# Optimization experiments

Measured on AMD Instinct MI355X. Metric: run time of the kernel, lower is better.

The kernel has to match this reference:

```python
import jax, jax.numpy as jnp
import numpy as np

B, S, D, E, K = 4, 2048, 1024, 8, 2
H = 4 * D  # SwiGLU hidden size


def setup_inputs() -> dict:
    key = jax.random.key(0)
    ks = jax.random.split(key, 6)
    s = 0.02
    return {
        "x": jax.random.normal(ks[0], (B, S, D), dtype=jnp.float32),
        "Wr": jax.random.normal(ks[1], (D, E), dtype=jnp.float32) * s,
        "br": jnp.zeros((E,), jnp.float32),
        "Wg": jax.random.normal(ks[2], (E, D, H), dtype=jnp.float32) * s,
        "bg": jnp.zeros((E, H), jnp.float32),
        "Wu": jax.random.normal(ks[3], (E, D, H), dtype=jnp.float32) * s,
        "bu": jnp.zeros((E, H), jnp.float32),
        "Wd": jax.random.normal(ks[4], (E, H, D), dtype=jnp.float32) * s,
        "bd": jnp.zeros((E, D), jnp.float32),
        "top_k": K,
    }


def reference(x, Wr, br, Wg, bg, Wu, bu, Wd, bd, top_k):
    # Router: top-k over expert logits, softmax over the selected k values.
    Bx, Sx, Dx = x.shape
    Ex = Wr.shape[-1]
    logits = x @ Wr + br                              # [B,S,E]
    vals, idx = jax.lax.top_k(logits, top_k)          # [B,S,K]
    probs = jax.nn.softmax(vals, axis=-1)             # [B,S,K]
    # Dense per-token expert weight; 0 for experts the token is not routed to.
    gate_w = jnp.sum(jax.nn.one_hot(idx, Ex, dtype=x.dtype) * probs[..., None], axis=-2)  # [B,S,E]

    xt = x.reshape(-1, Dx)          # [T,D]
    gw = gate_w.reshape(-1, Ex).T   # [E,T]

    def body(acc, p):
        wg, bgi, wu, bui, wd, bdi, ge = p
        h = jax.nn.silu(xt @ wg + bgi) * (xt @ wu + bui)   # [T,4D]
        y = (h @ wd + bdi) * ge[:, None]                   # zero where ge==0 (not routed)
        return acc + y, None

    out, _ = jax.lax.scan(body, jnp.zeros_like(xt), (Wg, bg, Wu, bu, Wd, bd, gw))
    return out.reshape(Bx, Sx, Dx)
```

## Files before the change

kernel.cpp:

```cpp
#include <hip/hip_runtime.h>
#include <hip/hip_fp16.h>


#define T_TOK 8192
#define D_IN  1024
#define E_EXP 8
#define H_HID 4096
#define NSLOT (T_TOK * 2)
#define NSLOT_PAD (NSLOT + 256)

typedef _Float16 f16;
typedef __attribute__((ext_vector_type(8))) _Float16 f16x8;
typedef __attribute__((ext_vector_type(4))) _Float16 f16x4;
typedef __attribute__((ext_vector_type(4))) float f32x4;

__device__ __forceinline__ void gload_lds16(const void* g, void* l) {
  __builtin_amdgcn_global_load_lds(
      (const __attribute__((address_space(1))) unsigned int*)g,
      (__attribute__((address_space(3))) unsigned int*)l, 16, 0, 0);
}


__global__ __launch_bounds__(256) void convert_x_kernel(
    const float* __restrict__ x, f16* __restrict__ xb, int n4) {
  int i = blockIdx.x * 256 + threadIdx.x;
  if (i >= n4) return;
  float4 v = ((const float4*)x)[i];
  f16x4 o = {(f16)v.x, (f16)v.y, (f16)v.z, (f16)v.w};
  *(f16x4*)(xb + (size_t)i * 4) = o;
}

template<int MAP>
__global__ __launch_bounds__(256) void transpose_cvt_kernel(
    const float* __restrict__ src, f16* __restrict__ dst, int R, int C,
    size_t dstride) {
  __shared__ float tile[32][33];
  int b = blockIdx.z;
  const float* s = src + (size_t)b * R * C;
  f16* d = dst + (size_t)b * dstride;
  int c0 = blockIdx.x * 32, r0 = blockIdx.y * 32;
  int tr = threadIdx.x >> 3;
  int tc4 = (threadIdx.x & 7) * 4;
  float4 v = *(const float4*)(s + (size_t)(r0 + tr) * C + c0 + tc4);
  tile[tr][tc4 + 0] = v.x;
  tile[tr][tc4 + 1] = v.y;
  tile[tr][tc4 + 2] = v.z;
  tile[tr][tc4 + 3] = v.w;
  __syncthreads();
  int c = c0 + tr;
  int ro = (MAP == 0) ? c : (((c >> 4) << 5) + ((MAP == 2) ? 16 : 0) + (c & 15));
  f16x4 o = {(f16)tile[tc4 + 0][tr], (f16)tile[tc4 + 1][tr],
             (f16)tile[tc4 + 2][tr], (f16)tile[tc4 + 3][tr]};
  *(f16x4*)(d + (size_t)ro * R + r0 + tc4) = o;
}


__global__ __launch_bounds__(256) void router_kernel(
    const float* __restrict__ x, const float* __restrict__ Wr,
    const float* __restrict__ br, int* __restrict__ eidx,
    float2* __restrict__ pval, int* __restrict__ counts) {
  int lane = threadIdx.x & 63, wid = threadIdx.x >> 6;
  int t = blockIdx.x * 4 + wid;
  const float* xr = x + (size_t)t * D_IN;
  float s[8] = {0.f, 0.f, 0.f, 0.f, 0.f, 0.f, 0.f, 0.f};
  int dbase = lane * 16;
#pragma unroll
  for (int i = 0; i < 4; ++i) {
    float4 xv = *(const float4*)(xr + dbase + i * 4);
    const float xs[4] = {xv.x, xv.y, xv.z, xv.w};
#pragma unroll
    for (int j = 0; j < 4; ++j) {
      const float* wr = Wr + (size_t)(dbase + i * 4 + j) * E_EXP;
      float4 w0 = *(const float4*)wr;
      float4 w1 = *(const float4*)(wr + 4);
      float xvj = xs[j];
      s[0] += xvj * w0.x; s[1] += xvj * w0.y; s[2] += xvj * w0.z; s[3] += xvj * w0.w;
      s[4] += xvj * w1.x; s[5] += xvj * w1.y; s[6] += xvj * w1.z; s[7] += xvj * w1.w;
    }
  }
#pragma unroll
  for (int off = 32; off; off >>= 1)
#pragma unroll
    for (int e = 0; e < 8; ++e) s[e] += __shfl_xor(s[e], off);
  if (lane == 0) {
    float v[8];
#pragma unroll
    for (int e = 0; e < 8; ++e) v[e] = s[e] + br[e];
    int i0 = 0; float v0 = v[0];
#pragma unroll
    for (int e = 1; e < 8; ++e) if (v[e] > v0) { v0 = v[e]; i0 = e; }
    int i1 = -1; float v1 = -1e30f;
#pragma unroll
    for (int e = 0; e < 8; ++e)
      if (e != i0 && v[e] > v1) { v1 = v[e]; i1 = e; }
    float ed = __expf(v1 - v0);
    float inv = 1.f / (1.f + ed);
    eidx[t] = i0 | (i1 << 8);
    pval[t] = make_float2(inv, ed * inv);
    atomicAdd(&counts[i0], 1);
    atomicAdd(&counts[i1], 1);
  }
}

__global__ void scan_kernel(const int* __restrict__ counts, int* __restrict__ offsets) {
  if (threadIdx.x == 0) {
    int acc = 0;
#pragma unroll
    for (int e = 0; e < E_EXP; ++e) { offsets[e] = acc; acc += counts[e]; }
    offsets[E_EXP] = acc;
  }
}

__global__ __launch_bounds__(256) void scatter_kernel(
    const int* __restrict__ eidx, const float2* __restrict__ pval,
    const int* __restrict__ offsets, int* __restrict__ cursors,
    int* __restrict__ perm, float* __restrict__ gatew, int2* __restrict__ slotAB) {
  int t = blockIdx.x * 256 + threadIdx.x;
  if (t >= T_TOK) return;
  int ei = eidx[t];
  float2 p = pval[t];
  int e0 = ei & 0xff, e1 = (ei >> 8) & 0xff;
  int s0 = offsets[e0] + atomicAdd(&cursors[e0], 1);
  perm[s0] = t; gatew[s0] = p.x;
  int s1 = offsets[e1] + atomicAdd(&cursors[e1], 1);
  perm[s1] = t; gatew[s1] = p.y;
  slotAB[t] = make_int2(s0, s1);
}


#define SB0 __builtin_amdgcn_sched_barrier(0)
#define BAR do { SB0; __builtin_amdgcn_s_barrier(); SB0; } while (0)

#define STAGE_(B, ISB, H, KT, BASE) do {                                   \
  char* d_ = smem + (B)*65536 + (ISB)*32768 + (H)*16384 + wid*1024;        \
  gload_lds16(BASE[(H)*2+0] + (size_t)(KT)*64, d_);                        \
  gload_lds16(BASE[(H)*2+1] + (size_t)(KT)*64, d_ + 8192);                 \
} while (0)

#define LDA_(B, Q)                                                          \
  _Pragma("unroll")                                                         \
  for (int m_ = 0; m_ < 4; ++m_) {                                          \
    fa[m_][0] = *(const f16x8*)(smem + (B)*65536 + aoff + ((Q)*4+m_)*2048 + offk0); \
    fa[m_][1] = *(const f16x8*)(smem + (B)*65536 + aoff + ((Q)*4+m_)*2048 + offk1); \
  }

#define LDB_(FB, B, RH)                                                     \
  _Pragma("unroll")                                                         \
  for (int n_ = 0; n_ < 2; ++n_) {                                          \
    FB[n_][0] = *(const f16x8*)(smem + (B)*65536 + 32768 + boff + ((RH)*2+n_)*2048 + offk0); \
    FB[n_][1] = *(const f16x8*)(smem + (B)*65536 + 32768 + boff + ((RH)*2+n_)*2048 + offk1); \
  }

#define QUAD_(Q, RH, FB)                                                    \
  __builtin_amdgcn_s_setprio(1);                                            \
  _Pragma("unroll")                                                         \
  for (int m_ = 0; m_ < 4; ++m_)                                            \
    _Pragma("unroll")                                                       \
    for (int n_ = 0; n_ < 2; ++n_) {                                        \
      acc[(Q)*4+m_][(RH)*2+n_] = __builtin_amdgcn_mfma_f32_16x16x32_f16(    \
          fa[m_][0], FB[n_][0], acc[(Q)*4+m_][(RH)*2+n_], 0, 0, 0);         \
      acc[(Q)*4+m_][(RH)*2+n_] = __builtin_amdgcn_mfma_f32_16x16x32_f16(    \
          fa[m_][1], FB[n_][1], acc[(Q)*4+m_][(RH)*2+n_], 0, 0, 0);         \
    }                                                                       \
  __builtin_amdgcn_s_setprio(0);

template<int MODE>
__global__ __launch_bounds__(512, 2) void ffn_8ph_kernel(
    const f16* __restrict__ Asrc, const f16* __restrict__ Bsrc,
    const float* __restrict__ bias0, const float* __restrict__ bias1,
    const int* __restrict__ offsets, const int* __restrict__ perm,
    const float* __restrict__ gatew, f16* __restrict__ dst) {
  constexpr int KD = MODE ? H_HID : D_IN;
  constexpr int BROWS = MODE ? D_IN : 2 * H_HID;
  constexpr int NT = KD / 64;
  static_assert(NT % 2 == 0, "NT even");

  __shared__ __align__(16) char smem[131072];

  int g = blockIdx.x;
  int xcd = g & 7;
  int mt = (g >> 3) & 31;
  int panel = xcd + 8 * (g >> 8);
  int e, nt;
  if constexpr (MODE == 0) { e = panel >> 5; nt = panel & 31; }
  else                     { e = panel >> 2; nt = panel & 3; }

  int off = offsets[e];
  int cnt = offsets[e + 1] - off;
  if (mt * 256 >= cnt) return;

  int tid = threadIdx.x, lane = tid & 63, wid = tid >> 6;
  int wm = wid >> 2, wn = wid & 3;
  int l15 = lane & 15, lc0 = lane >> 4, s7 = l15 & 7;
  int aoff = (wm * 128 + l15) * 128;
  int boff = (wn * 64 + l15) * 128;
  int offk0 = ((lc0) ^ s7) * 16;
  int offk1 = ((lc0 + 4) ^ s7) * 16;

  int rowh_[2], lc_[2];
#pragma unroll
  for (int i = 0; i < 2; ++i) {
    int chunk = (i * 8 + wid) * 64 + lane;
    rowh_[i] = chunk >> 3;
    lc_[i] = (chunk & 7) ^ (rowh_[i] & 7);
  }

  const f16 *aB[4], *bB[4];
#pragma unroll
  for (int h = 0; h < 2; ++h)
#pragma unroll
    for (int i = 0; i < 2; ++i) {
      int absrow = h * 128 + rowh_[i];
      bB[h * 2 + i] =
          Bsrc + ((size_t)e * BROWS + nt * 256 + absrow) * KD + lc_[i] * 8;
      int slot = off + min(mt * 256 + absrow, cnt - 1);
      if constexpr (MODE == 0)
        aB[h * 2 + i] = Asrc + (size_t)perm[slot] * KD + lc_[i] * 8;
      else
        aB[h * 2 + i] = Asrc + (size_t)slot * KD + lc_[i] * 8;
    }

  float bv0[4], bv1[2];
  if constexpr (MODE == 0) {
#pragma unroll
    for (int p = 0; p < 2; ++p) {
      int h = nt * 128 + wn * 32 + p * 16 + l15;
      bv0[p] = bias0[e * H_HID + h];
      bv1[p] = bias1[e * H_HID + h];
    }
  } else {
#pragma unroll
    for (int n = 0; n < 4; ++n)
      bv0[n] = bias0[e * D_IN + nt * 256 + wn * 64 + n * 16 + l15];
  }

  f32x4 acc[8][4] = {};
  f16x8 fa[4][2], fb01[2][2], fb23[2][2];

  STAGE_(0, 1, 0, 0, bB); STAGE_(0, 1, 1, 0, bB);
  STAGE_(0, 0, 0, 0, aB); STAGE_(0, 0, 1, 0, aB);
  STAGE_(1, 1, 0, 1, bB); STAGE_(1, 1, 1, 1, bB);
  asm volatile("s_waitcnt vmcnt(4)" ::: "memory");
  BAR;

  for (int it = 0; it < NT / 2; ++it) {
    int t1 = 2 * it + 1;
    int t2 = min(2 * it + 2, NT - 1);
    int t3 = min(2 * it + 3, NT - 1);
    LDA_(0, 0); LDB_(fb01, 0, 0); STAGE_(1, 0, 0, t1, aB);
    BAR; QUAD_(0, 0, fb01); BAR;
    LDB_(fb23, 0, 1); STAGE_(1, 0, 1, t1, aB);
    BAR; QUAD_(0, 1, fb23); BAR;
    LDA_(0, 1); STAGE_(0, 1, 0, t2, bB);
    BAR; QUAD_(1, 0, fb01); BAR;
    STAGE_(0, 1, 1, t2, bB);
    asm volatile("s_waitcnt vmcnt(4)" ::: "memory");
    BAR; QUAD_(1, 1, fb23); BAR;
    LDA_(1, 0); LDB_(fb01, 1, 0); STAGE_(0, 0, 0, t2, aB);
    BAR; QUAD_(0, 0, fb01); BAR;
    LDB_(fb23, 1, 1); STAGE_(0, 0, 1, t2, aB);
    BAR; QUAD_(0, 1, fb23); BAR;
    LDA_(1, 1); STAGE_(1, 1, 0, t3, bB);
    BAR; QUAD_(1, 0, fb01); BAR;
    STAGE_(1, 1, 1, t3, bB);
    asm volatile("s_waitcnt vmcnt(4)" ::: "memory");
    BAR; QUAD_(1, 1, fb23); BAR;
  }

  asm volatile("s_waitcnt vmcnt(0)" ::: "memory");
  BAR;

  int c0_ = lc0 * 4;
  if constexpr (MODE == 0) {
#pragma unroll
    for (int p = 0; p < 2; ++p) {
      int h = nt * 128 + wn * 32 + p * 16 + l15;
#pragma unroll
      for (int m = 0; m < 8; ++m) {
        int lbase = mt * 256 + wm * 128 + m * 16 + c0_;
#pragma unroll
        for (int r = 0; r < 4; ++r) {
          if (lbase + r < cnt) {
            float gv = acc[m][2 * p][r] + bv0[p];
            float uv = acc[m][2 * p + 1][r] + bv1[p];
            __builtin_nontemporal_store(
                (f16)((gv / (1.f + __expf(-gv))) * uv),
                &dst[(size_t)(off + lbase + r) * H_HID + h]);
          }
        }
      }
    }
  } else {
#pragma unroll
    for (int n = 0; n < 4; ++n) {
      int col = nt * 256 + wn * 64 + n * 16 + l15;
#pragma unroll
      for (int m = 0; m < 8; ++m) {
        int lbase = mt * 256 + wm * 128 + m * 16 + c0_;
#pragma unroll
        for (int r = 0; r < 4; ++r) {
          if (lbase + r < cnt) {
            int slot = off + lbase + r;
            __builtin_nontemporal_store(
                (f16)(gatew[slot] * (acc[m][n][r] + bv0[n])),
                &dst[(size_t)slot * D_IN + col]);
          }
        }
      }
    }
  }
}

__global__ __launch_bounds__(256) void combine_kernel(
    const f16* __restrict__ ybuf, const int2* __restrict__ slotAB,
    float* __restrict__ out) {
  int i = blockIdx.x * 256 + threadIdx.x;
  int t = i >> 7;
  int c8 = i & 127;
  int2 s = slotAB[t];
  f16x8 y0 = *(const f16x8*)(ybuf + (size_t)s.x * D_IN + c8 * 8);
  f16x8 y1 = *(const f16x8*)(ybuf + (size_t)s.y * D_IN + c8 * 8);
  float* o = out + (size_t)t * D_IN + c8 * 8;
  f32x4 o0 = {(float)y0[0] + (float)y1[0], (float)y0[1] + (float)y1[1],
              (float)y0[2] + (float)y1[2], (float)y0[3] + (float)y1[3]};
  f32x4 o1 = {(float)y0[4] + (float)y1[4], (float)y0[5] + (float)y1[5],
              (float)y0[6] + (float)y1[6], (float)y0[7] + (float)y1[7]};
  __builtin_nontemporal_store(o0, (f32x4*)o);
  __builtin_nontemporal_store(o1, (f32x4*)(o + 4));
}


extern "C" void kernel_launch(void* const* d_in, const int* in_sizes, int n_in,
                              void* d_out, int out_size, void* d_ws, size_t ws_size,
                              hipStream_t stream) {
  const float* x  = (const float*)d_in[0];
  const float* Wr = (const float*)d_in[1];
  const float* br = (const float*)d_in[2];
  const float* Wg = (const float*)d_in[3];
  const float* bg = (const float*)d_in[4];
  const float* Wu = (const float*)d_in[5];
  const float* bu = (const float*)d_in[6];
  const float* Wd = (const float*)d_in[7];
  const float* bd = (const float*)d_in[8];
  float* out = (float*)d_out;

  char* ws = (char*)d_ws;
  size_t o = 0;
  auto alloc = [&](size_t bytes) {
    size_t r = o;
    o += (bytes + 255) & ~(size_t)255;
    return r;
  };
  f16* xb     = (f16*)(ws + alloc((size_t)T_TOK * D_IN * 2));
  f16* wgut   = (f16*)(ws + alloc((size_t)E_EXP * 2 * H_HID * D_IN * 2));
  f16* wdt    = (f16*)(ws + alloc((size_t)E_EXP * D_IN * H_HID * 2));
  f16* hbuf   = (f16*)(ws + alloc((size_t)NSLOT_PAD * H_HID * 2));
  int* eidx   = (int*)(ws + alloc((size_t)T_TOK * 4));
  float2* pval= (float2*)(ws + alloc((size_t)T_TOK * 8));
  int* counts = (int*)(ws + alloc(64 * 4));
  int* cursors = counts + 8;
  int* offsets = counts + 16;
  int* perm   = (int*)(ws + alloc((size_t)NSLOT_PAD * 4));
  float* gatew= (float*)(ws + alloc((size_t)NSLOT_PAD * 4));
  int2* slotAB= (int2*)(ws + alloc((size_t)T_TOK * 8));
  f16* ybuf   = wgut;

  hipMemsetAsync(counts, 0, 64 * 4, stream);

  convert_x_kernel<<<(T_TOK * D_IN / 4 + 255) / 256, 256, 0, stream>>>(
      x, xb, T_TOK * D_IN / 4);
  router_kernel<<<T_TOK / 4, 256, 0, stream>>>(x, Wr, br, eidx, pval, counts);
  scan_kernel<<<1, 64, 0, stream>>>(counts, offsets);
  scatter_kernel<<<T_TOK / 256, 256, 0, stream>>>(eidx, pval, offsets, cursors,
                                                  perm, gatew, slotAB);
  transpose_cvt_kernel<1><<<dim3(H_HID / 32, D_IN / 32, E_EXP), 256, 0, stream>>>(
      Wg, wgut, D_IN, H_HID, (size_t)2 * H_HID * D_IN);
  transpose_cvt_kernel<2><<<dim3(H_HID / 32, D_IN / 32, E_EXP), 256, 0, stream>>>(
      Wu, wgut, D_IN, H_HID, (size_t)2 * H_HID * D_IN);
  ffn_8ph_kernel<0><<<dim3(8192), 512, 0, stream>>>(
      xb, wgut, bg, bu, offsets, perm, nullptr, hbuf);
  transpose_cvt_kernel<0><<<dim3(D_IN / 32, H_HID / 32, E_EXP), 256, 0, stream>>>(
      Wd, wdt, H_HID, D_IN, (size_t)D_IN * H_HID);
  ffn_8ph_kernel<1><<<dim3(1024), 512, 0, stream>>>(
      hbuf, wdt, bd, nullptr, offsets, nullptr, gatew, ybuf);
  combine_kernel<<<T_TOK * D_IN / 8 / 256, 256, 0, stream>>>(ybuf, slotAB, out);
}
```

Baseline: 1.012 ms.

## Fuse x conversion into router and deepen GEMM load prefetch schedule

Removes the separate fp32-to-fp16 conversion kernel for x by having the router write the fp16 copy while it reads x, saving a launch and one extra read of x. Also reorders the staged global-to-LDS loads in the expert GEMM main loop so the next A half-tile is issued a step earlier. The waitcnt points are moved to match, and the trailing vmcnt(0) drain is removed. This gives more latency hiding for the loads, at the cost of more outstanding loads and a subtler correctness dependence on the waitcnt counts.

```diff
diff --git a/kernel.cpp b/kernel.cpp
--- a/kernel.cpp
+++ b/kernel.cpp
@@ -18,16 +18,6 @@
   __builtin_amdgcn_global_load_lds(
       (const __attribute__((address_space(1))) unsigned int*)g,
       (__attribute__((address_space(3))) unsigned int*)l, 16, 0, 0);
-}
-
-
-__global__ __launch_bounds__(256) void convert_x_kernel(
-    const float* __restrict__ x, f16* __restrict__ xb, int n4) {
-  int i = blockIdx.x * 256 + threadIdx.x;
-  if (i >= n4) return;
-  float4 v = ((const float4*)x)[i];
-  f16x4 o = {(f16)v.x, (f16)v.y, (f16)v.z, (f16)v.w};
-  *(f16x4*)(xb + (size_t)i * 4) = o;
 }
 
 template<int MAP>
@@ -58,7 +48,8 @@
 __global__ __launch_bounds__(256) void router_kernel(
     const float* __restrict__ x, const float* __restrict__ Wr,
     const float* __restrict__ br, int* __restrict__ eidx,
-    float2* __restrict__ pval, int* __restrict__ counts) {
+    float2* __restrict__ pval, int* __restrict__ counts,
+    f16* __restrict__ xb) {
   int lane = threadIdx.x & 63, wid = threadIdx.x >> 6;
   int t = blockIdx.x * 4 + wid;
   const float* xr = x + (size_t)t * D_IN;
@@ -67,6 +58,8 @@
 #pragma unroll
   for (int i = 0; i < 4; ++i) {
     float4 xv = *(const float4*)(xr + dbase + i * 4);
+    f16x4 xo = {(f16)xv.x, (f16)xv.y, (f16)xv.z, (f16)xv.w};
+    *(f16x4*)(xb + (size_t)t * D_IN + dbase + i * 4) = xo;
     const float xs[4] = {xv.x, xv.y, xv.z, xv.w};
 #pragma unroll
     for (int j = 0; j < 4; ++j) {
@@ -130,6 +123,7 @@
 
 #define SB0 __builtin_amdgcn_sched_barrier(0)
 #define BAR do { SB0; __builtin_amdgcn_s_barrier(); SB0; } while (0)
+#define VMCNT(N) asm volatile("s_waitcnt vmcnt(" #N ")" ::: "memory")
 
 #define STAGE_(B, ISB, H, KT, BASE) do {                                   \
   char* d_ = smem + (B)*65536 + (ISB)*32768 + (H)*16384 + wid*1024;        \
@@ -240,35 +234,35 @@
   STAGE_(0, 1, 0, 0, bB); STAGE_(0, 1, 1, 0, bB);
   STAGE_(0, 0, 0, 0, aB); STAGE_(0, 0, 1, 0, aB);
   STAGE_(1, 1, 0, 1, bB); STAGE_(1, 1, 1, 1, bB);
-  asm volatile("s_waitcnt vmcnt(4)" ::: "memory");
+  STAGE_(1, 0, 0, 1, aB);
+  VMCNT(6);
   BAR;
 
   for (int it = 0; it < NT / 2; ++it) {
-    int t1 = 2 * it + 1;
-    int t2 = min(2 * it + 2, NT - 1);
-    int t3 = min(2 * it + 3, NT - 1);
-    LDA_(0, 0); LDB_(fb01, 0, 0); STAGE_(1, 0, 0, t1, aB);
+    int b_ = 2 * it + 1;
+    int a2 = min(2 * it + 2, NT - 1);
+    int b2 = min(2 * it + 3, NT - 1);
+    LDA_(0, 0); LDB_(fb01, 0, 0); STAGE_(1, 0, 1, b_, aB);
     BAR; QUAD_(0, 0, fb01); BAR;
-    LDB_(fb23, 0, 1); STAGE_(1, 0, 1, t1, aB);
+    LDB_(fb23, 0, 1);
     BAR; QUAD_(0, 1, fb23); BAR;
-    LDA_(0, 1); STAGE_(0, 1, 0, t2, bB);
+    LDA_(0, 1); STAGE_(0, 1, 0, a2, bB);
     BAR; QUAD_(1, 0, fb01); BAR;
-    STAGE_(0, 1, 1, t2, bB);
-    asm volatile("s_waitcnt vmcnt(4)" ::: "memory");
-    BAR; QUAD_(1, 1, fb23); BAR;
-    LDA_(1, 0); LDB_(fb01, 1, 0); STAGE_(0, 0, 0, t2, aB);
+    STAGE_(0, 1, 1, a2, bB);
+    BAR; QUAD_(1, 1, fb23);
+    VMCNT(4);
+    BAR;
+    LDA_(1, 0); LDB_(fb01, 1, 0); STAGE_(0, 0, 0, a2, aB);
     BAR; QUAD_(0, 0, fb01); BAR;
-    LDB_(fb23, 1, 1); STAGE_(0, 0, 1, t2, aB);
+    LDB_(fb23, 1, 1); STAGE_(0, 0, 1, a2, aB);
     BAR; QUAD_(0, 1, fb23); BAR;
-    LDA_(1, 1); STAGE_(1, 1, 0, t3, bB);
+    LDA_(1, 1); STAGE_(1, 1, 0, b2, bB);
     BAR; QUAD_(1, 0, fb01); BAR;
-    STAGE_(1, 1, 1, t3, bB);
-    asm volatile("s_waitcnt vmcnt(4)" ::: "memory");
-    BAR; QUAD_(1, 1, fb23); BAR;
-  }
-
-  asm volatile("s_waitcnt vmcnt(0)" ::: "memory");
-  BAR;
+    STAGE_(1, 1, 1, b2, bB); STAGE_(1, 0, 0, b2, aB);
+    BAR; QUAD_(1, 1, fb23);
+    VMCNT(6);
+    BAR;
+  }
 
   int c0_ = lc0 * 4;
   if constexpr (MODE == 0) {
@@ -367,9 +361,7 @@
 
   hipMemsetAsync(counts, 0, 64 * 4, stream);
 
-  convert_x_kernel<<<(T_TOK * D_IN / 4 + 255) / 256, 256, 0, stream>>>(
-      x, xb, T_TOK * D_IN / 4);
-  router_kernel<<<T_TOK / 4, 256, 0, stream>>>(x, Wr, br, eidx, pval, counts);
+  router_kernel<<<T_TOK / 4, 256, 0, stream>>>(x, Wr, br, eidx, pval, counts, xb);
   scan_kernel<<<1, 64, 0, stream>>>(counts, offsets);
   scatter_kernel<<<T_TOK / 256, 256, 0, stream>>>(eidx, pval, offsets, cursors,
                                                   perm, gatew, slotAB);
```

Measured after the change: 1.003 ms. No clear change (-0.9%).
